# Optimization experiments

Measured on AMD Instinct MI355X. Metric: run time of the kernel, lower is better.

Reference implementation:

```python
import jax, jax.numpy as jnp
import numpy as np

EPS = 1e-5

def _neighbor_idx(H, W):
    # flat index of the 3x3 clamped neighborhood for each pixel, [H*W, 9]
    r = np.arange(H)[:, None, None]  # [H,1,1]
    c = np.arange(W)[None, :, None]  # [1,W,1]
    dr = np.repeat(np.array([-1, 0, 1]), 3)[None, None, :]  # [1,1,9]
    dc = np.tile(np.array([-1, 0, 1]), 3)[None, None, :]
    ri = np.clip(r + dr, 0, H - 1)
    ci = np.clip(c + dc, 0, W - 1)
    return jnp.asarray((ri * W + ci).reshape(H * W, 9))

def setup_inputs() -> dict:
    key = jax.random.key(0)
    ks = jax.random.split(key, 7)
    B, C, H, W = 16, 256, 80, 80
    s = 1.0 / np.sqrt(C)
    return {
        "x": jax.random.normal(ks[0], (B, C, H, W), jnp.float32),
        "Wq": jax.random.normal(ks[1], (C, C), jnp.float32) * s,
        "bq": jax.random.normal(ks[2], (C,), jnp.float32) * s,
        "Wk": jax.random.normal(ks[3], (C, C), jnp.float32) * s,
        "bk": jax.random.normal(ks[4], (C,), jnp.float32) * s,
        "Wv": jax.random.normal(ks[5], (C, C), jnp.float32) * s,
        "bv": jax.random.normal(ks[6], (C,), jnp.float32) * s,
    }

def reference(x, Wq, bq, Wk, bk, Wv, bv):
    B, C, H, W = x.shape
    N = H * W
    xf = x.reshape(B, C, N)
    # 1x1 convs as channel GEMMs
    q = jnp.einsum('oc,bcn->bno', Wq, xf) + bq          # [B,N,C]
    k = jnp.einsum('oc,bcn->bon', Wk, xf) + bk[:, None]  # [B,C,N]
    v = jnp.einsum('oc,bcn->bon', Wv, xf) + bv[:, None]  # [B,C,N]
    idx = _neighbor_idx(H, W)                            # [N,9]
    k_n = k[:, :, idx]                                   # [B,C,N,9]
    v_n = v[:, :, idx]                                   # [B,C,N,9]
    # raw attention scores (NOT softmaxed before AV, matching the source)
    scores = jnp.einsum('bnc,bcnq->bnq', q, k_n)         # [B,N,9]
    new_v = jnp.einsum('bnq,bcnq->bcn', scores, v_n).reshape(B, C, H, W)
    out9 = scores.reshape(B, H, W, 9)
    center = out9[..., 4]
    others_mean = (out9.sum(-1) - center) / 8.0
    output = jnp.stack([center, others_mean], axis=-1)   # [B,H,W,2]
    # residual + layer_norm over [H,W] (no affine), per (B,C)
    xr = x + new_v
    mu = xr.mean(axis=(-2, -1), keepdims=True)
    var = ((xr - mu) ** 2).mean(axis=(-2, -1), keepdims=True)
    x_out = (xr - mu) * jax.lax.rsqrt(var + EPS)
    return (output, x_out)
```

## Files before the change

### kernel.cpp

```cpp
#include <hip/hip_runtime.h>
#include <hip/hip_bf16.h>

using f32x4  = __attribute__((ext_vector_type(4))) float;
using short8 = __attribute__((ext_vector_type(8))) short;
using bf16   = __hip_bfloat16;

constexpr int BATCH = 16;
constexpr int CH    = 256;
constexpr int HH    = 80;
constexpr int WW    = 80;
constexpr int NPIX  = HH * WW;

__device__ __forceinline__ float b2f(unsigned short u) {
    union { unsigned int i; float f; } x;
    x.i = ((unsigned int)u) << 16;
    return x.f;
}

__global__ __launch_bounds__(256) void convert_w(
    const float* __restrict__ Wq, const float* __restrict__ Wk,
    const float* __restrict__ Wv, bf16* __restrict__ Wb)
{
    const int elem = blockIdx.x * 256 + threadIdx.x;
    const int mat  = blockIdx.y;
    const float* src = (mat == 0) ? Wq : (mat == 1) ? Wk : Wv;
    Wb[(size_t)mat * CH * CH + elem] = __float2bfloat16(src[elem]);
}

__global__ __launch_bounds__(256) void transpose_cast(
    const float* __restrict__ x, bf16* __restrict__ xt, int b0)
{
    __shared__ float t[64][65];
    const int b  = b0 + blockIdx.z;
    const int n0 = blockIdx.x * 64;
    const int c0 = blockIdx.y * 64;
    const float* xb = x + (size_t)b * CH * NPIX;
    const int tid = threadIdx.x;

    {
        const int nl  = tid & 63;
        const int cl0 = tid >> 6;
        #pragma unroll
        for (int i = 0; i < 16; ++i) {
            const int cl = cl0 + i * 4;
            t[cl][nl] = xb[(size_t)(c0 + cl) * NPIX + n0 + nl];
        }
    }
    __syncthreads();
    {
        bf16* xtb = xt + (size_t)blockIdx.z * NPIX * CH;
        const int cl  = tid & 63;
        const int nl0 = tid >> 6;
        #pragma unroll
        for (int i = 0; i < 16; ++i) {
            const int nl = nl0 + i * 4;
            xtb[(size_t)(n0 + nl) * CH + c0 + cl] = __float2bfloat16(t[cl][nl]);
        }
    }
}

__global__ __launch_bounds__(256) void qkv_mfma(
    const bf16* __restrict__ xt, const bf16* __restrict__ Wb,
    const float* __restrict__ bq, const float* __restrict__ bk,
    const float* __restrict__ bv,
    bf16* __restrict__ qo, bf16* __restrict__ ko, bf16* __restrict__ vt)
{
    const int m  = blockIdx.z % 3;
    const int bl = blockIdx.z / 3;
    const int n0 = blockIdx.x * 128;
    const int o0 = blockIdx.y * 128;
    const bf16*  W    = Wb + (size_t)m * CH * CH;
    const float* bias = (m == 0) ? bq : (m == 1) ? bk : bv;
    const bf16*  A    = xt + (size_t)bl * NPIX * CH;

    __shared__ short As[128 * 36];
    __shared__ short Bs[128 * 36];

    const int tid = threadIdx.x;
    const int wv  = tid >> 6, ln = tid & 63;
    const int wr  = wv >> 1,  wc = wv & 1;
    const int lm  = ln & 15,  lk = ln >> 4;

    f32x4 acc[4][4];
    #pragma unroll
    for (int i = 0; i < 4; ++i)
        #pragma unroll
        for (int j = 0; j < 4; ++j)
            #pragma unroll
            for (int r = 0; r < 4; ++r) acc[i][j][r] = 0.f;

    for (int k0 = 0; k0 < CH; k0 += 32) {
        #pragma unroll
        for (int it = 0; it < 2; ++it) {
            const int q   = tid + it * 256;
            const int row = q >> 2, ch = q & 3;
            const int4 av = *(const int4*)(A + (size_t)(n0 + row) * CH + k0 + ch * 8);
            *(int4*)((char*)As + row * 72 + ch * 16) = av;
            const int4 wvv = *(const int4*)(W + (size_t)(o0 + row) * CH + k0 + ch * 8);
            *(int4*)((char*)Bs + row * 72 + ch * 16) = wvv;
        }
        __syncthreads();

        short8 afr[4], bfr[4];
        #pragma unroll
        for (int i = 0; i < 4; ++i) {
            const int row = wr * 64 + i * 16 + lm;
            afr[i] = *(const short8*)((const char*)As + row * 72 + lk * 16);
        }
        #pragma unroll
        for (int j = 0; j < 4; ++j) {
            const int row = wc * 64 + j * 16 + lm;
            bfr[j] = *(const short8*)((const char*)Bs + row * 72 + lk * 16);
        }
        #pragma unroll
        for (int i = 0; i < 4; ++i)
            #pragma unroll
            for (int j = 0; j < 4; ++j)
                acc[i][j] = __builtin_amdgcn_mfma_f32_16x16x32_bf16(
                    afr[i], bfr[j], acc[i][j], 0, 0, 0);
        __syncthreads();
    }

    if (m < 2) {
        bf16* out = (m == 0 ? qo : ko) + (size_t)bl * NPIX * CH;
        #pragma unroll
        for (int j = 0; j < 4; ++j) {
            const int o = o0 + wc * 64 + j * 16 + lm;
            const float bs = bias[o];
            #pragma unroll
            for (int i = 0; i < 4; ++i) {
                const int nb = n0 + wr * 64 + i * 16 + lk * 4;
                #pragma unroll
                for (int r = 0; r < 4; ++r)
                    out[(size_t)(nb + r) * CH + o] = __float2bfloat16(acc[i][j][r] + bs);
            }
        }
    } else {
        bf16* out = vt + (size_t)bl * CH * NPIX;
        #pragma unroll
        for (int j = 0; j < 4; ++j) {
            const int o = o0 + wc * 64 + j * 16 + lm;
            const float bs = bias[o];
            #pragma unroll
            for (int i = 0; i < 4; ++i) {
                const int nb = n0 + wr * 64 + i * 16 + lk * 4;
                ushort4 pk;
                #pragma unroll
                for (int r = 0; r < 4; ++r) {
                    const bf16 h = __float2bfloat16(acc[i][j][r] + bs);
                    ((unsigned short*)&pk)[r] = *(const unsigned short*)&h;
                }
                *(ushort4*)((bf16*)out + (size_t)o * NPIX + nb) = pk;
            }
        }
    }
}

__global__ __launch_bounds__(256) void scores_kernel(
    const bf16* __restrict__ q, const bf16* __restrict__ k,
    float* __restrict__ scores, float* __restrict__ out0, int b0)
{
    const int wave = threadIdx.x >> 6, lane = threadIdx.x & 63;
    const int n  = blockIdx.x * 4 + wave;
    const int bl = blockIdx.y;
    const int b  = b0 + bl;

    const unsigned short* qrow = (const unsigned short*)(q + ((size_t)bl * NPIX + n) * CH) + lane * 4;
    const unsigned short* kb   = (const unsigned short*)(k + (size_t)bl * NPIX * CH);

    const ushort4 qu = *(const ushort4*)qrow;
    const float q0 = b2f(qu.x), q1 = b2f(qu.y), q2 = b2f(qu.z), q3 = b2f(qu.w);

    const int r = n / WW, col = n % WW;
    float s[9], ssum = 0.f;
    #pragma unroll
    for (int j = 0; j < 9; ++j) {
        const int rr = min(max(r + j / 3 - 1, 0), HH - 1);
        const int c2 = min(max(col + j % 3 - 1, 0), WW - 1);
        const int nbr = rr * WW + c2;
        const ushort4 kv = *(const ushort4*)(kb + (size_t)nbr * CH + lane * 4);
        float d = q0 * b2f(kv.x) + q1 * b2f(kv.y) + q2 * b2f(kv.z) + q3 * b2f(kv.w);
        #pragma unroll
        for (int off = 32; off >= 1; off >>= 1) d += __shfl_xor(d, off, 64);
        s[j] = d;
        ssum += d;
    }
    if (lane == 0) {
        float* sp = scores + ((size_t)bl * NPIX + n) * 9;
        #pragma unroll
        for (int j = 0; j < 9; ++j) sp[j] = s[j];
        const float center = s[4];
        out0[((size_t)b * NPIX + n) * 2 + 0] = center;
        out0[((size_t)b * NPIX + n) * 2 + 1] = (ssum - center) * 0.125f;
    }
}

__global__ __launch_bounds__(256) void newv_ln(
    const float* __restrict__ x, const bf16* __restrict__ vt,
    const float* __restrict__ scores, float* __restrict__ xout, int b0)
{
    const int c  = blockIdx.x;
    const int bl = blockIdx.y;
    const int b  = b0 + bl;
    const int tid = threadIdx.x;

    const unsigned short* vrow = (const unsigned short*)(vt + ((size_t)bl * CH + c) * NPIX);
    const float* xrow = x + ((size_t)b * CH + c) * NPIX;
    const float* sb   = scores + (size_t)bl * NPIX * 9;

    float val[25];
    float sum = 0.f, sq = 0.f;
    #pragma unroll
    for (int it = 0; it < 25; ++it) {
        const int n   = tid + it * 256;
        const int r   = n / WW;
        const int col = n - r * WW;
        const float* sp = sb + (size_t)n * 9;
        const int rm = max(r - 1, 0) * WW;
        const int r0 = r * WW;
        const int rp = min(r + 1, HH - 1) * WW;
        const int cm = max(col - 1, 0);
        const int cp = min(col + 1, WW - 1);
        float a;
        a  = sp[0] * b2f(vrow[rm + cm]) + sp[1] * b2f(vrow[rm + col]) + sp[2] * b2f(vrow[rm + cp]);
        a += sp[3] * b2f(vrow[r0 + cm]) + sp[4] * b2f(vrow[r0 + col]) + sp[5] * b2f(vrow[r0 + cp]);
        a += sp[6] * b2f(vrow[rp + cm]) + sp[7] * b2f(vrow[rp + col]) + sp[8] * b2f(vrow[rp + cp]);
        const float vv = xrow[n] + a;
        val[it] = vv;
        sum += vv;
        sq  += vv * vv;
    }

    #pragma unroll
    for (int off = 32; off >= 1; off >>= 1) {
        sum += __shfl_xor(sum, off, 64);
        sq  += __shfl_xor(sq,  off, 64);
    }
    __shared__ float rs[4], rq[4];
    const int wave = tid >> 6, lane = tid & 63;
    if (lane == 0) { rs[wave] = sum; rq[wave] = sq; }
    __syncthreads();
    sum = rs[0] + rs[1] + rs[2] + rs[3];
    sq  = rq[0] + rq[1] + rq[2] + rq[3];

    const float mu   = sum * (1.f / NPIX);
    const float var  = sq * (1.f / NPIX) - mu * mu;
    const float rstd = rsqrtf(var + 1e-5f);

    float* orow = xout + ((size_t)b * CH + c) * NPIX;
    #pragma unroll
    for (int it = 0; it < 25; ++it) {
        const int n = tid + it * 256;
        orow[n] = (val[it] - mu) * rstd;
    }
}

extern "C" void kernel_launch(void* const* d_in, const int* in_sizes, int n_in,
                              void* d_out, int out_size, void* d_ws, size_t ws_size,
                              hipStream_t stream)
{
    const float* x  = (const float*)d_in[0];
    const float* Wq = (const float*)d_in[1];
    const float* bq = (const float*)d_in[2];
    const float* Wk = (const float*)d_in[3];
    const float* bk = (const float*)d_in[4];
    const float* Wv = (const float*)d_in[5];
    const float* bv = (const float*)d_in[6];

    float* out0 = (float*)d_out;
    float* xout = out0 + (size_t)BATCH * NPIX * 2;

    char* ws = (char*)d_ws;
    bf16* Wb = (bf16*)ws;
    ws += (size_t)3 * CH * CH * sizeof(bf16);

    const size_t fBF = (size_t)NPIX * CH * sizeof(bf16);
    const size_t fSC = (size_t)NPIX * 9 * sizeof(float);
    const size_t perBatch = 4 * fBF + fSC;

    size_t avail = ws_size - ((size_t)3 * CH * CH * sizeof(bf16));
    int NB = (int)(avail / perBatch);
    if (NB < 1)  NB = 1;
    if (NB > BATCH) NB = BATCH;

    bf16*  xt  = (bf16*)ws;
    bf16*  qb  = (bf16*)(ws + (size_t)NB * fBF);
    bf16*  kb  = (bf16*)(ws + (size_t)NB * fBF * 2);
    bf16*  vt  = (bf16*)(ws + (size_t)NB * fBF * 3);
    float* sc  = (float*)(ws + (size_t)NB * fBF * 4);

    convert_w<<<dim3(CH * CH / 256, 3), 256, 0, stream>>>(Wq, Wk, Wv, Wb);

    for (int b0 = 0; b0 < BATCH; b0 += NB) {
        const int cnb = (BATCH - b0 < NB) ? (BATCH - b0) : NB;

        transpose_cast<<<dim3(NPIX / 64, CH / 64, cnb), 256, 0, stream>>>(x, xt, b0);

        qkv_mfma<<<dim3(NPIX / 128, CH / 128, cnb * 3), 256, 0, stream>>>(
            xt, Wb, bq, bk, bv, qb, kb, vt);

        scores_kernel<<<dim3(NPIX / 4, cnb), 256, 0, stream>>>(qb, kb, sc, out0, b0);

        newv_ln<<<dim3(CH, cnb), 256, 0, stream>>>(x, vt, sc, xout, b0);
    }
}
```

Before: 321.5 us.

## Vectorize q/k stores, transpose score layout, stage v row in LDS

The q/k GEMM swaps the MFMA operands so each lane holds four consecutive output channels, which lets it write packed 8-byte stores instead of scattered 2-byte ones. The scores buffer moves from a pixel-major [N][9] layout to a plane-major [9][N] layout. The newv+layernorm kernel now runs 320 threads, copies the bf16 v row into LDS, processes four pixels per thread with float4 loads of scores and x, and writes float4 outputs. This targets uncoalesced global traffic, at the cost of strided single-lane score writes in the scores kernel and a larger per-block LDS footprint.

```diff
diff --git a/kernel.cpp b/kernel.cpp
--- a/kernel.cpp
+++ b/kernel.cpp
@@ -112,12 +112,21 @@
             const int row = wc * 64 + j * 16 + lm;
             bfr[j] = *(const short8*)((const char*)Bs + row * 72 + lk * 16);
         }
-        #pragma unroll
-        for (int i = 0; i < 4; ++i)
-            #pragma unroll
-            for (int j = 0; j < 4; ++j)
-                acc[i][j] = __builtin_amdgcn_mfma_f32_16x16x32_bf16(
-                    afr[i], bfr[j], acc[i][j], 0, 0, 0);
+        if (m < 2) {
+            #pragma unroll
+            for (int i = 0; i < 4; ++i)
+                #pragma unroll
+                for (int j = 0; j < 4; ++j)
+                    acc[i][j] = __builtin_amdgcn_mfma_f32_16x16x32_bf16(
+                        bfr[j], afr[i], acc[i][j], 0, 0, 0);
+        } else {
+            #pragma unroll
+            for (int i = 0; i < 4; ++i)
+                #pragma unroll
+                for (int j = 0; j < 4; ++j)
+                    acc[i][j] = __builtin_amdgcn_mfma_f32_16x16x32_bf16(
+                        afr[i], bfr[j], acc[i][j], 0, 0, 0);
+        }
         __syncthreads();
     }
 
@@ -125,14 +134,23 @@
         bf16* out = (m == 0 ? qo : ko) + (size_t)bl * NPIX * CH;
         #pragma unroll
         for (int j = 0; j < 4; ++j) {
-            const int o = o0 + wc * 64 + j * 16 + lm;
-            const float bs = bias[o];
+            const int ob = o0 + wc * 64 + j * 16 + lk * 4;
+            const float4 b4 = *(const float4*)(bias + ob);
             #pragma unroll
             for (int i = 0; i < 4; ++i) {
-                const int nb = n0 + wr * 64 + i * 16 + lk * 4;
-                #pragma unroll
-                for (int r = 0; r < 4; ++r)
-                    out[(size_t)(nb + r) * CH + o] = __float2bfloat16(acc[i][j][r] + bs);
+                const int n = n0 + wr * 64 + i * 16 + lm;
+                ushort4 pk;
+                {
+                    const bf16 h0 = __float2bfloat16(acc[i][j][0] + b4.x);
+                    const bf16 h1 = __float2bfloat16(acc[i][j][1] + b4.y);
+                    const bf16 h2 = __float2bfloat16(acc[i][j][2] + b4.z);
+                    const bf16 h3 = __float2bfloat16(acc[i][j][3] + b4.w);
+                    pk.x = *(const unsigned short*)&h0;
+                    pk.y = *(const unsigned short*)&h1;
+                    pk.z = *(const unsigned short*)&h2;
+                    pk.w = *(const unsigned short*)&h3;
+                }
+                *(ushort4*)(out + (size_t)n * CH + ob) = pk;
             }
         }
     } else {
@@ -150,7 +168,7 @@
                     const bf16 h = __float2bfloat16(acc[i][j][r] + bs);
                     ((unsigned short*)&pk)[r] = *(const unsigned short*)&h;
                 }
-                *(ushort4*)((bf16*)out + (size_t)o * NPIX + nb) = pk;
+                *(ushort4*)(out + (size_t)o * NPIX + nb) = pk;
             }
         }
     }
@@ -186,19 +204,22 @@
         ssum += d;
     }
     if (lane == 0) {
-        float* sp = scores + ((size_t)bl * NPIX + n) * 9;
-        #pragma unroll
-        for (int j = 0; j < 9; ++j) sp[j] = s[j];
+        float* sp = scores + (size_t)bl * 9 * NPIX;
+        #pragma unroll
+        for (int j = 0; j < 9; ++j) sp[(size_t)j * NPIX + n] = s[j];
         const float center = s[4];
         out0[((size_t)b * NPIX + n) * 2 + 0] = center;
         out0[((size_t)b * NPIX + n) * 2 + 1] = (ssum - center) * 0.125f;
     }
 }
 
-__global__ __launch_bounds__(256) void newv_ln(
+__global__ __launch_bounds__(320) void newv_ln(
     const float* __restrict__ x, const bf16* __restrict__ vt,
     const float* __restrict__ scores, float* __restrict__ xout, int b0)
 {
+    __shared__ __align__(16) unsigned short lds_v[NPIX];
+    __shared__ float rsum[5], rsq[5];
+
     const int c  = blockIdx.x;
     const int bl = blockIdx.y;
     const int b  = b0 + bl;
@@ -206,29 +227,67 @@
 
     const unsigned short* vrow = (const unsigned short*)(vt + ((size_t)bl * CH + c) * NPIX);
     const float* xrow = x + ((size_t)b * CH + c) * NPIX;
-    const float* sb   = scores + (size_t)bl * NPIX * 9;
-
-    float val[25];
+    const float* sb   = scores + (size_t)bl * 9 * NPIX;
+
+    #pragma unroll
+    for (int i = 0; i < 3; ++i) {
+        const int t = tid + i * 320;
+        if (t < NPIX / 8) ((int4*)lds_v)[t] = ((const int4*)vrow)[t];
+    }
+    __syncthreads();
+
+    float val[20];
     float sum = 0.f, sq = 0.f;
     #pragma unroll
-    for (int it = 0; it < 25; ++it) {
-        const int n   = tid + it * 256;
-        const int r   = n / WW;
-        const int col = n - r * WW;
-        const float* sp = sb + (size_t)n * 9;
+    for (int it = 0; it < 5; ++it) {
+        const int p   = tid + it * 320;
+        const int n0  = p * 4;
+        const int r   = p / 20;
+        const int c0  = (p % 20) * 4;
+
         const int rm = max(r - 1, 0) * WW;
         const int r0 = r * WW;
         const int rp = min(r + 1, HH - 1) * WW;
-        const int cm = max(col - 1, 0);
-        const int cp = min(col + 1, WW - 1);
-        float a;
-        a  = sp[0] * b2f(vrow[rm + cm]) + sp[1] * b2f(vrow[rm + col]) + sp[2] * b2f(vrow[rm + cp]);
-        a += sp[3] * b2f(vrow[r0 + cm]) + sp[4] * b2f(vrow[r0 + col]) + sp[5] * b2f(vrow[r0 + cp]);
-        a += sp[6] * b2f(vrow[rp + cm]) + sp[7] * b2f(vrow[rp + col]) + sp[8] * b2f(vrow[rp + cp]);
-        const float vv = xrow[n] + a;
-        val[it] = vv;
-        sum += vv;
-        sq  += vv * vv;
+
+        float4 s[9];
+        #pragma unroll
+        for (int j = 0; j < 9; ++j)
+            s[j] = *(const float4*)(sb + (size_t)j * NPIX + n0);
+
+        const float4 xin = *(const float4*)(xrow + n0);
+
+        const int cA = max(c0 - 1, 0);
+        const int cF = min(c0 + 4, WW - 1);
+        float vm[6], v0[6], vp[6];
+        vm[0] = b2f(lds_v[rm + cA]); v0[0] = b2f(lds_v[r0 + cA]); vp[0] = b2f(lds_v[rp + cA]);
+        #pragma unroll
+        for (int t = 1; t < 5; ++t) {
+            vm[t] = b2f(lds_v[rm + c0 + t - 1]);
+            v0[t] = b2f(lds_v[r0 + c0 + t - 1]);
+            vp[t] = b2f(lds_v[rp + c0 + t - 1]);
+        }
+        vm[5] = b2f(lds_v[rm + cF]); v0[5] = b2f(lds_v[r0 + cF]); vp[5] = b2f(lds_v[rp + cF]);
+
+        #pragma unroll
+        for (int px = 0; px < 4; ++px) {
+            const float sc0 = ((const float*)&s[0])[px];
+            const float sc1 = ((const float*)&s[1])[px];
+            const float sc2 = ((const float*)&s[2])[px];
+            const float sc3 = ((const float*)&s[3])[px];
+            const float sc4 = ((const float*)&s[4])[px];
+            const float sc5 = ((const float*)&s[5])[px];
+            const float sc6 = ((const float*)&s[6])[px];
+            const float sc7 = ((const float*)&s[7])[px];
+            const float sc8 = ((const float*)&s[8])[px];
+            float a;
+            a  = sc0 * vm[px] + sc1 * vm[px + 1] + sc2 * vm[px + 2];
+            a += sc3 * v0[px] + sc4 * v0[px + 1] + sc5 * v0[px + 2];
+            a += sc6 * vp[px] + sc7 * vp[px + 1] + sc8 * vp[px + 2];
+            const float vv = ((const float*)&xin)[px] + a;
+            val[it * 4 + px] = vv;
+            sum += vv;
+            sq  += vv * vv;
+        }
     }
 
     #pragma unroll
@@ -236,12 +295,11 @@
         sum += __shfl_xor(sum, off, 64);
         sq  += __shfl_xor(sq,  off, 64);
     }
-    __shared__ float rs[4], rq[4];
     const int wave = tid >> 6, lane = tid & 63;
-    if (lane == 0) { rs[wave] = sum; rq[wave] = sq; }
+    if (lane == 0) { rsum[wave] = sum; rsq[wave] = sq; }
     __syncthreads();
-    sum = rs[0] + rs[1] + rs[2] + rs[3];
-    sq  = rq[0] + rq[1] + rq[2] + rq[3];
+    sum = rsum[0] + rsum[1] + rsum[2] + rsum[3] + rsum[4];
+    sq  = rsq[0]  + rsq[1]  + rsq[2]  + rsq[3]  + rsq[4];
 
     const float mu   = sum * (1.f / NPIX);
     const float var  = sq * (1.f / NPIX) - mu * mu;
@@ -249,9 +307,14 @@
 
     float* orow = xout + ((size_t)b * CH + c) * NPIX;
     #pragma unroll
-    for (int it = 0; it < 25; ++it) {
-        const int n = tid + it * 256;
-        orow[n] = (val[it] - mu) * rstd;
+    for (int it = 0; it < 5; ++it) {
+        const int n0 = (tid + it * 320) * 4;
+        float4 o;
+        o.x = (val[it * 4 + 0] - mu) * rstd;
+        o.y = (val[it * 4 + 1] - mu) * rstd;
+        o.z = (val[it * 4 + 2] - mu) * rstd;
+        o.w = (val[it * 4 + 3] - mu) * rstd;
+        *(float4*)(orow + n0) = o;
     }
 }
 
@@ -301,6 +364,6 @@
 
         scores_kernel<<<dim3(NPIX / 4, cnb), 256, 0, stream>>>(qb, kb, sc, out0, b0);
 
-        newv_ln<<<dim3(CH, cnb), 256, 0, stream>>>(x, vt, sc, xout, b0);
-    }
-}
+        newv_ln<<<dim3(CH, cnb), 320, 0, stream>>>(x, vt, sc, xout, b0);
+    }
+}
```

New measurement: 326.7 us. No clear change (+1.6%).
